# Kernel optimization log

Hardware: AMD Instinct MI355X
Metric: run time of the kernel (lower is better)

The kernel has to match this reference:

```python
import jax, jax.numpy as jnp
import numpy as np

B, S, D, E, K = 4, 2048, 1024, 8, 2
H = 4 * D  # SwiGLU hidden size


def setup_inputs() -> dict:
    key = jax.random.key(0)
    ks = jax.random.split(key, 6)
    s = 0.02
    return {
        "x": jax.random.normal(ks[0], (B, S, D), dtype=jnp.float32),
        "Wr": jax.random.normal(ks[1], (D, E), dtype=jnp.float32) * s,
        "br": jnp.zeros((E,), jnp.float32),
        "Wg": jax.random.normal(ks[2], (E, D, H), dtype=jnp.float32) * s,
        "bg": jnp.zeros((E, H), jnp.float32),
        "Wu": jax.random.normal(ks[3], (E, D, H), dtype=jnp.float32) * s,
        "bu": jnp.zeros((E, H), jnp.float32),
        "Wd": jax.random.normal(ks[4], (E, H, D), dtype=jnp.float32) * s,
        "bd": jnp.zeros((E, D), jnp.float32),
        "top_k": K,
    }


def reference(x, Wr, br, Wg, bg, Wu, bu, Wd, bd, top_k):
    # Router: top-k over expert logits, softmax over the selected k values.
    Bx, Sx, Dx = x.shape
    Ex = Wr.shape[-1]
    logits = x @ Wr + br                              # [B,S,E]
    vals, idx = jax.lax.top_k(logits, top_k)          # [B,S,K]
    probs = jax.nn.softmax(vals, axis=-1)             # [B,S,K]
    # Dense per-token expert weight; 0 for experts the token is not routed to.
    gate_w = jnp.sum(jax.nn.one_hot(idx, Ex, dtype=x.dtype) * probs[..., None], axis=-2)  # [B,S,E]

    xt = x.reshape(-1, Dx)          # [T,D]
    gw = gate_w.reshape(-1, Ex).T   # [E,T]

    def body(acc, p):
        wg, bgi, wu, bui, wd, bdi, ge = p
        h = jax.nn.silu(xt @ wg + bgi) * (xt @ wu + bui)   # [T,4D]
        y = (h @ wd + bdi) * ge[:, None]                   # zero where ge==0 (not routed)
        return acc + y, None

    out, _ = jax.lax.scan(body, jnp.zeros_like(xt), (Wg, bg, Wu, bu, Wd, bd, gw))
    return out.reshape(Bx, Sx, Dx)
```

## Files before the change

kernel.cpp:

```cpp
#include <hip/hip_runtime.h>
#include <hip/hip_fp16.h>


#define T_TOK 8192
#define D_IN  1024
#define E_EXP 8
#define H_HID 4096
#define NSLOT (T_TOK * 2)
#define NSLOT_PAD (NSLOT + 256)

typedef _Float16 f16;
typedef __attribute__((ext_vector_type(8))) _Float16 f16x8;
typedef __attribute__((ext_vector_type(4))) _Float16 f16x4;
typedef __attribute__((ext_vector_type(4))) float f32x4;

__device__ __forceinline__ void gload_lds16(const void* g, void* l) {
  __builtin_amdgcn_global_load_lds(
      (const __attribute__((address_space(1))) unsigned int*)g,
      (__attribute__((address_space(3))) unsigned int*)l, 16, 0, 0);
}


__global__ __launch_bounds__(256) void convert_x_kernel(
    const float* __restrict__ x, f16* __restrict__ xb, int n4) {
  int i = blockIdx.x * 256 + threadIdx.x;
  if (i >= n4) return;
  float4 v = ((const float4*)x)[i];
  f16x4 o = {(f16)v.x, (f16)v.y, (f16)v.z, (f16)v.w};
  *(f16x4*)(xb + (size_t)i * 4) = o;
}

template<int MAP>
__global__ __launch_bounds__(256) void transpose_cvt_kernel(
    const float* __restrict__ src, f16* __restrict__ dst, int R, int C,
    size_t dstride) {
  __shared__ float tile[32][33];
  int b = blockIdx.z;
  const float* s = src + (size_t)b * R * C;
  f16* d = dst + (size_t)b * dstride;
  int c0 = blockIdx.x * 32, r0 = blockIdx.y * 32;
  int tr = threadIdx.x >> 3;
  int tc4 = (threadIdx.x & 7) * 4;
  float4 v = *(const float4*)(s + (size_t)(r0 + tr) * C + c0 + tc4);
  tile[tr][tc4 + 0] = v.x;
  tile[tr][tc4 + 1] = v.y;
  tile[tr][tc4 + 2] = v.z;
  tile[tr][tc4 + 3] = v.w;
  __syncthreads();
  int c = c0 + tr;
  int ro = (MAP == 0) ? c : (((c >> 4) << 5) + ((MAP == 2) ? 16 : 0) + (c & 15));
  f16x4 o = {(f16)tile[tc4 + 0][tr], (f16)tile[tc4 + 1][tr],
             (f16)tile[tc4 + 2][tr], (f16)tile[tc4 + 3][tr]};
  *(f16x4*)(d + (size_t)ro * R + r0 + tc4) = o;
}


__global__ __launch_bounds__(256) void router_kernel(
    const float* __restrict__ x, const float* __restrict__ Wr,
    const float* __restrict__ br, int* __restrict__ eidx,
    float2* __restrict__ pval, int* __restrict__ counts) {
  int lane = threadIdx.x & 63, wid = threadIdx.x >> 6;
  int t = blockIdx.x * 4 + wid;
  const float* xr = x + (size_t)t * D_IN;
  float s[8] = {0.f, 0.f, 0.f, 0.f, 0.f, 0.f, 0.f, 0.f};
  int dbase = lane * 16;
#pragma unroll
  for (int i = 0; i < 4; ++i) {
    float4 xv = *(const float4*)(xr + dbase + i * 4);
    const float xs[4] = {xv.x, xv.y, xv.z, xv.w};
#pragma unroll
    for (int j = 0; j < 4; ++j) {
      const float* wr = Wr + (size_t)(dbase + i * 4 + j) * E_EXP;
      float4 w0 = *(const float4*)wr;
      float4 w1 = *(const float4*)(wr + 4);
      float xvj = xs[j];
      s[0] += xvj * w0.x; s[1] += xvj * w0.y; s[2] += xvj * w0.z; s[3] += xvj * w0.w;
      s[4] += xvj * w1.x; s[5] += xvj * w1.y; s[6] += xvj * w1.z; s[7] += xvj * w1.w;
    }
  }
#pragma unroll
  for (int off = 32; off; off >>= 1)
#pragma unroll
    for (int e = 0; e < 8; ++e) s[e] += __shfl_xor(s[e], off);
  if (lane == 0) {
    float v[8];
#pragma unroll
    for (int e = 0; e < 8; ++e) v[e] = s[e] + br[e];
    int i0 = 0; float v0 = v[0];
#pragma unroll
    for (int e = 1; e < 8; ++e) if (v[e] > v0) { v0 = v[e]; i0 = e; }
    int i1 = -1; float v1 = -1e30f;
#pragma unroll
    for (int e = 0; e < 8; ++e)
      if (e != i0 && v[e] > v1) { v1 = v[e]; i1 = e; }
    float ed = __expf(v1 - v0);
    float inv = 1.f / (1.f + ed);
    eidx[t] = i0 | (i1 << 8);
    pval[t] = make_float2(inv, ed * inv);
    atomicAdd(&counts[i0], 1);
    atomicAdd(&counts[i1], 1);
  }
}

__global__ void scan_kernel(const int* __restrict__ counts, int* __restrict__ offsets) {
  if (threadIdx.x == 0) {
    int acc = 0;
#pragma unroll
    for (int e = 0; e < E_EXP; ++e) { offsets[e] = acc; acc += counts[e]; }
    offsets[E_EXP] = acc;
  }
}

__global__ __launch_bounds__(256) void scatter_kernel(
    const int* __restrict__ eidx, const float2* __restrict__ pval,
    const int* __restrict__ offsets, int* __restrict__ cursors,
    int* __restrict__ perm, float* __restrict__ gatew, int2* __restrict__ slotAB) {
  int t = blockIdx.x * 256 + threadIdx.x;
  if (t >= T_TOK) return;
  int ei = eidx[t];
  float2 p = pval[t];
  int e0 = ei & 0xff, e1 = (ei >> 8) & 0xff;
  int s0 = offsets[e0] + atomicAdd(&cursors[e0], 1);
  perm[s0] = t; gatew[s0] = p.x;
  int s1 = offsets[e1] + atomicAdd(&cursors[e1], 1);
  perm[s1] = t; gatew[s1] = p.y;
  slotAB[t] = make_int2(s0, s1);
}


#define SB0 __builtin_amdgcn_sched_barrier(0)
#define BAR do { SB0; __builtin_amdgcn_s_barrier(); SB0; } while (0)

#define STAGE_(B, ISB, H, KT, BASE) do {                                   \
  char* d_ = smem + (B)*65536 + (ISB)*32768 + (H)*16384 + wid*1024;        \
  gload_lds16(BASE[(H)*2+0] + (size_t)(KT)*64, d_);                        \
  gload_lds16(BASE[(H)*2+1] + (size_t)(KT)*64, d_ + 8192);                 \
} while (0)

#define LDA_(B, Q)                                                          \
  _Pragma("unroll")                                                         \
  for (int m_ = 0; m_ < 4; ++m_) {                                          \
    fa[m_][0] = *(const f16x8*)(smem + (B)*65536 + aoff + ((Q)*4+m_)*2048 + offk0); \
    fa[m_][1] = *(const f16x8*)(smem + (B)*65536 + aoff + ((Q)*4+m_)*2048 + offk1); \
  }

#define LDB_(FB, B, RH)                                                     \
  _Pragma("unroll")                                                         \
  for (int n_ = 0; n_ < 2; ++n_) {                                          \
    FB[n_][0] = *(const f16x8*)(smem + (B)*65536 + 32768 + boff + ((RH)*2+n_)*2048 + offk0); \
    FB[n_][1] = *(const f16x8*)(smem + (B)*65536 + 32768 + boff + ((RH)*2+n_)*2048 + offk1); \
  }

#define QUAD_(Q, RH, FB)                                                    \
  __builtin_amdgcn_s_setprio(1);                                            \
  _Pragma("unroll")                                                         \
  for (int m_ = 0; m_ < 4; ++m_)                                            \
    _Pragma("unroll")                                                       \
    for (int n_ = 0; n_ < 2; ++n_) {                                        \
      acc[(Q)*4+m_][(RH)*2+n_] = __builtin_amdgcn_mfma_f32_16x16x32_f16(    \
          fa[m_][0], FB[n_][0], acc[(Q)*4+m_][(RH)*2+n_], 0, 0, 0);         \
      acc[(Q)*4+m_][(RH)*2+n_] = __builtin_amdgcn_mfma_f32_16x16x32_f16(    \
          fa[m_][1], FB[n_][1], acc[(Q)*4+m_][(RH)*2+n_], 0, 0, 0);         \
    }                                                                       \
  __builtin_amdgcn_s_setprio(0);

template<int MODE>
__global__ __launch_bounds__(512, 2) void ffn_8ph_kernel(
    const f16* __restrict__ Asrc, const f16* __restrict__ Bsrc,
    const float* __restrict__ bias0, const float* __restrict__ bias1,
    const int* __restrict__ offsets, const int* __restrict__ perm,
    const float* __restrict__ gatew, f16* __restrict__ dst) {
  constexpr int KD = MODE ? H_HID : D_IN;
  constexpr int BROWS = MODE ? D_IN : 2 * H_HID;
  constexpr int NT = KD / 64;
  static_assert(NT % 2 == 0, "NT even");

  __shared__ __align__(16) char smem[131072];

  int nt = blockIdx.x, e = blockIdx.y, mt = blockIdx.z;
  int off = offsets[e];
  int cnt = offsets[e + 1] - off;
  if (mt * 256 >= cnt) return;

  int tid = threadIdx.x, lane = tid & 63, wid = tid >> 6;
  int wm = wid >> 2, wn = wid & 3;
  int l15 = lane & 15, lc0 = lane >> 4, s7 = l15 & 7;
  int aoff = (wm * 128 + l15) * 128;
  int boff = (wn * 64 + l15) * 128;
  int offk0 = ((lc0) ^ s7) * 16;
  int offk1 = ((lc0 + 4) ^ s7) * 16;

  const f16 *aB[4], *bB[4];
#pragma unroll
  for (int h = 0; h < 2; ++h)
#pragma unroll
    for (int i = 0; i < 2; ++i) {
      int chunk = (i * 8 + wid) * 64 + lane;
      int rowh = chunk >> 3;
      int lc = (chunk & 7) ^ (rowh & 7);
      int absrow = h * 128 + rowh;
      int slot = off + min(mt * 256 + absrow, cnt - 1);
      if constexpr (MODE == 0)
        aB[h * 2 + i] = Asrc + (size_t)perm[slot] * KD + lc * 8;
      else
        aB[h * 2 + i] = Asrc + (size_t)slot * KD + lc * 8;
      bB[h * 2 + i] = Bsrc + ((size_t)e * BROWS + nt * 256 + absrow) * KD + lc * 8;
    }

  f32x4 acc[8][4] = {};
  f16x8 fa[4][2], fb01[2][2], fb23[2][2];

  STAGE_(0, 1, 0, 0, bB); STAGE_(0, 1, 1, 0, bB);
  STAGE_(0, 0, 0, 0, aB); STAGE_(0, 0, 1, 0, aB);
  STAGE_(1, 1, 0, 1, bB); STAGE_(1, 1, 1, 1, bB);
  asm volatile("s_waitcnt vmcnt(4)" ::: "memory");
  BAR;

  for (int it = 0; it < NT / 2; ++it) {
    int t1 = 2 * it + 1;
    int t2 = min(2 * it + 2, NT - 1);
    int t3 = min(2 * it + 3, NT - 1);
    LDA_(0, 0); LDB_(fb01, 0, 0); STAGE_(1, 0, 0, t1, aB);
    BAR; QUAD_(0, 0, fb01); BAR;
    LDB_(fb23, 0, 1); STAGE_(1, 0, 1, t1, aB);
    BAR; QUAD_(0, 1, fb23); BAR;
    LDA_(0, 1); STAGE_(0, 1, 0, t2, bB);
    BAR; QUAD_(1, 0, fb01); BAR;
    STAGE_(0, 1, 1, t2, bB);
    asm volatile("s_waitcnt vmcnt(4)" ::: "memory");
    BAR; QUAD_(1, 1, fb23); BAR;
    LDA_(1, 0); LDB_(fb01, 1, 0); STAGE_(0, 0, 0, t2, aB);
    BAR; QUAD_(0, 0, fb01); BAR;
    LDB_(fb23, 1, 1); STAGE_(0, 0, 1, t2, aB);
    BAR; QUAD_(0, 1, fb23); BAR;
    LDA_(1, 1); STAGE_(1, 1, 0, t3, bB);
    BAR; QUAD_(1, 0, fb01); BAR;
    STAGE_(1, 1, 1, t3, bB);
    asm volatile("s_waitcnt vmcnt(4)" ::: "memory");
    BAR; QUAD_(1, 1, fb23); BAR;
  }

  asm volatile("s_waitcnt vmcnt(0)" ::: "memory");
  BAR;

  int c0_ = lc0 * 4;
  if constexpr (MODE == 0) {
#pragma unroll
    for (int p = 0; p < 2; ++p) {
      int h = nt * 128 + wn * 32 + p * 16 + l15;
      float bgv = bias0[e * H_HID + h];
      float buv = bias1[e * H_HID + h];
#pragma unroll
      for (int m = 0; m < 8; ++m) {
        int lbase = mt * 256 + wm * 128 + m * 16 + c0_;
#pragma unroll
        for (int r = 0; r < 4; ++r) {
          if (lbase + r < cnt) {
            float g = acc[m][2 * p][r] + bgv;
            float u = acc[m][2 * p + 1][r] + buv;
            dst[(size_t)(off + lbase + r) * H_HID + h] =
                (f16)((g / (1.f + __expf(-g))) * u);
          }
        }
      }
    }
  } else {
#pragma unroll
    for (int n = 0; n < 4; ++n) {
      int col = nt * 256 + wn * 64 + n * 16 + l15;
      float bdv = bias0[e * D_IN + col];
#pragma unroll
      for (int m = 0; m < 8; ++m) {
        int lbase = mt * 256 + wm * 128 + m * 16 + c0_;
#pragma unroll
        for (int r = 0; r < 4; ++r) {
          if (lbase + r < cnt) {
            int slot = off + lbase + r;
            dst[(size_t)slot * D_IN + col] = (f16)(gatew[slot] * (acc[m][n][r] + bdv));
          }
        }
      }
    }
  }
}

__global__ __launch_bounds__(256) void combine_kernel(
    const f16* __restrict__ ybuf, const int2* __restrict__ slotAB,
    float* __restrict__ out) {
  int i = blockIdx.x * 256 + threadIdx.x;
  int t = i >> 7;
  int c8 = i & 127;
  int2 s = slotAB[t];
  f16x8 y0 = *(const f16x8*)(ybuf + (size_t)s.x * D_IN + c8 * 8);
  f16x8 y1 = *(const f16x8*)(ybuf + (size_t)s.y * D_IN + c8 * 8);
  float* o = out + (size_t)t * D_IN + c8 * 8;
  float4 o0 = make_float4((float)y0[0] + (float)y1[0], (float)y0[1] + (float)y1[1],
                          (float)y0[2] + (float)y1[2], (float)y0[3] + (float)y1[3]);
  float4 o1 = make_float4((float)y0[4] + (float)y1[4], (float)y0[5] + (float)y1[5],
                          (float)y0[6] + (float)y1[6], (float)y0[7] + (float)y1[7]);
  ((float4*)o)[0] = o0;
  ((float4*)o)[1] = o1;
}


extern "C" void kernel_launch(void* const* d_in, const int* in_sizes, int n_in,
                              void* d_out, int out_size, void* d_ws, size_t ws_size,
                              hipStream_t stream) {
  const float* x  = (const float*)d_in[0];
  const float* Wr = (const float*)d_in[1];
  const float* br = (const float*)d_in[2];
  const float* Wg = (const float*)d_in[3];
  const float* bg = (const float*)d_in[4];
  const float* Wu = (const float*)d_in[5];
  const float* bu = (const float*)d_in[6];
  const float* Wd = (const float*)d_in[7];
  const float* bd = (const float*)d_in[8];
  float* out = (float*)d_out;

  char* ws = (char*)d_ws;
  size_t o = 0;
  auto alloc = [&](size_t bytes) {
    size_t r = o;
    o += (bytes + 255) & ~(size_t)255;
    return r;
  };
  f16* xb     = (f16*)(ws + alloc((size_t)T_TOK * D_IN * 2));
  f16* wgut   = (f16*)(ws + alloc((size_t)E_EXP * 2 * H_HID * D_IN * 2));
  f16* wdt    = (f16*)(ws + alloc((size_t)E_EXP * D_IN * H_HID * 2));
  f16* hbuf   = (f16*)(ws + alloc((size_t)NSLOT_PAD * H_HID * 2));
  int* eidx   = (int*)(ws + alloc((size_t)T_TOK * 4));
  float2* pval= (float2*)(ws + alloc((size_t)T_TOK * 8));
  int* counts = (int*)(ws + alloc(64 * 4));
  int* cursors = counts + 8;
  int* offsets = counts + 16;
  int* perm   = (int*)(ws + alloc((size_t)NSLOT_PAD * 4));
  float* gatew= (float*)(ws + alloc((size_t)NSLOT_PAD * 4));
  int2* slotAB= (int2*)(ws + alloc((size_t)T_TOK * 8));
  f16* ybuf   = wgut;

  hipMemsetAsync(counts, 0, 64 * 4, stream);

  convert_x_kernel<<<(T_TOK * D_IN / 4 + 255) / 256, 256, 0, stream>>>(
      x, xb, T_TOK * D_IN / 4);
  transpose_cvt_kernel<1><<<dim3(H_HID / 32, D_IN / 32, E_EXP), 256, 0, stream>>>(
      Wg, wgut, D_IN, H_HID, (size_t)2 * H_HID * D_IN);
  transpose_cvt_kernel<2><<<dim3(H_HID / 32, D_IN / 32, E_EXP), 256, 0, stream>>>(
      Wu, wgut, D_IN, H_HID, (size_t)2 * H_HID * D_IN);
  transpose_cvt_kernel<0><<<dim3(D_IN / 32, H_HID / 32, E_EXP), 256, 0, stream>>>(
      Wd, wdt, H_HID, D_IN, (size_t)D_IN * H_HID);
  router_kernel<<<T_TOK / 4, 256, 0, stream>>>(x, Wr, br, eidx, pval, counts);
  scan_kernel<<<1, 64, 0, stream>>>(counts, offsets);
  scatter_kernel<<<T_TOK / 256, 256, 0, stream>>>(eidx, pval, offsets, cursors,
                                                  perm, gatew, slotAB);
  ffn_8ph_kernel<0><<<dim3(2 * H_HID / 256, E_EXP, 32), 512, 0, stream>>>(
      xb, wgut, bg, bu, offsets, perm, nullptr, hbuf);
  ffn_8ph_kernel<1><<<dim3(D_IN / 256, E_EXP, 32), 512, 0, stream>>>(
      hbuf, wdt, bd, nullptr, offsets, nullptr, gatew, ybuf);
  combine_kernel<<<T_TOK * D_IN / 8 / 256, 256, 0, stream>>>(ybuf, slotAB, out);
}
```

Before: 1.054 ms.

## Make gate/up FFN persistent per expert column tile and XCD-swizzle down-proj grid

The gate/up kernel now launches one block per (expert, N-tile), 256 blocks in total. Each block loops over all of that expert's M tiles, replacing the old 3D grid that launched many early-exiting blocks. The down-projection kernel uses a flat 1024-block grid whose index is remapped so that blocks sharing an expert's weight tiles land on the same XCD, which should improve L2 reuse. Biases are hoisted out of the M loop. The risk is load imbalance: each gate/up block runs serially over a variable number of tiles, so a heavily loaded expert sets the critical path.

```diff
diff --git a/kernel.cpp b/kernel.cpp
--- a/kernel.cpp
+++ b/kernel.cpp
@@ -177,10 +177,20 @@
 
   __shared__ __align__(16) char smem[131072];
 
-  int nt = blockIdx.x, e = blockIdx.y, mt = blockIdx.z;
+  int e, nt, mt0, mt1;
+  int g = blockIdx.x;
+  if constexpr (MODE == 0) {
+    e = g >> 5; nt = g & 31;
+  } else {
+    int xcd = g & 7, r = g >> 3;
+    int pair = xcd + 8 * (r & 3);
+    e = pair >> 2; nt = pair & 3; mt0 = r >> 2;
+  }
   int off = offsets[e];
   int cnt = offsets[e + 1] - off;
-  if (mt * 256 >= cnt) return;
+  int ntiles = (cnt + 255) >> 8;
+  if constexpr (MODE == 0) { mt0 = 0; mt1 = ntiles; }
+  else { if (mt0 >= ntiles) return; mt1 = mt0 + 1; }
 
   int tid = threadIdx.x, lane = tid & 63, wid = tid >> 6;
   int wm = wid >> 2, wn = wid & 3;
@@ -190,93 +200,119 @@
   int offk0 = ((lc0) ^ s7) * 16;
   int offk1 = ((lc0 + 4) ^ s7) * 16;
 
-  const f16 *aB[4], *bB[4];
+  int rowh_[2], lc_[2];
+#pragma unroll
+  for (int i = 0; i < 2; ++i) {
+    int chunk = (i * 8 + wid) * 64 + lane;
+    rowh_[i] = chunk >> 3;
+    lc_[i] = (chunk & 7) ^ (rowh_[i] & 7);
+  }
+
+  const f16* bB[4];
 #pragma unroll
   for (int h = 0; h < 2; ++h)
 #pragma unroll
-    for (int i = 0; i < 2; ++i) {
-      int chunk = (i * 8 + wid) * 64 + lane;
-      int rowh = chunk >> 3;
-      int lc = (chunk & 7) ^ (rowh & 7);
-      int absrow = h * 128 + rowh;
-      int slot = off + min(mt * 256 + absrow, cnt - 1);
-      if constexpr (MODE == 0)
-        aB[h * 2 + i] = Asrc + (size_t)perm[slot] * KD + lc * 8;
-      else
-        aB[h * 2 + i] = Asrc + (size_t)slot * KD + lc * 8;
-      bB[h * 2 + i] = Bsrc + ((size_t)e * BROWS + nt * 256 + absrow) * KD + lc * 8;
-    }
-
-  f32x4 acc[8][4] = {};
-  f16x8 fa[4][2], fb01[2][2], fb23[2][2];
-
-  STAGE_(0, 1, 0, 0, bB); STAGE_(0, 1, 1, 0, bB);
-  STAGE_(0, 0, 0, 0, aB); STAGE_(0, 0, 1, 0, aB);
-  STAGE_(1, 1, 0, 1, bB); STAGE_(1, 1, 1, 1, bB);
-  asm volatile("s_waitcnt vmcnt(4)" ::: "memory");
-  BAR;
-
-  for (int it = 0; it < NT / 2; ++it) {
-    int t1 = 2 * it + 1;
-    int t2 = min(2 * it + 2, NT - 1);
-    int t3 = min(2 * it + 3, NT - 1);
-    LDA_(0, 0); LDB_(fb01, 0, 0); STAGE_(1, 0, 0, t1, aB);
-    BAR; QUAD_(0, 0, fb01); BAR;
-    LDB_(fb23, 0, 1); STAGE_(1, 0, 1, t1, aB);
-    BAR; QUAD_(0, 1, fb23); BAR;
-    LDA_(0, 1); STAGE_(0, 1, 0, t2, bB);
-    BAR; QUAD_(1, 0, fb01); BAR;
-    STAGE_(0, 1, 1, t2, bB);
-    asm volatile("s_waitcnt vmcnt(4)" ::: "memory");
-    BAR; QUAD_(1, 1, fb23); BAR;
-    LDA_(1, 0); LDB_(fb01, 1, 0); STAGE_(0, 0, 0, t2, aB);
-    BAR; QUAD_(0, 0, fb01); BAR;
-    LDB_(fb23, 1, 1); STAGE_(0, 0, 1, t2, aB);
-    BAR; QUAD_(0, 1, fb23); BAR;
-    LDA_(1, 1); STAGE_(1, 1, 0, t3, bB);
-    BAR; QUAD_(1, 0, fb01); BAR;
-    STAGE_(1, 1, 1, t3, bB);
-    asm volatile("s_waitcnt vmcnt(4)" ::: "memory");
-    BAR; QUAD_(1, 1, fb23); BAR;
-  }
-
-  asm volatile("s_waitcnt vmcnt(0)" ::: "memory");
-  BAR;
-
-  int c0_ = lc0 * 4;
+    for (int i = 0; i < 2; ++i)
+      bB[h * 2 + i] =
+          Bsrc + ((size_t)e * BROWS + nt * 256 + h * 128 + rowh_[i]) * KD + lc_[i] * 8;
+
+  float bv0[4], bv1[2];
   if constexpr (MODE == 0) {
 #pragma unroll
     for (int p = 0; p < 2; ++p) {
       int h = nt * 128 + wn * 32 + p * 16 + l15;
-      float bgv = bias0[e * H_HID + h];
-      float buv = bias1[e * H_HID + h];
-#pragma unroll
-      for (int m = 0; m < 8; ++m) {
-        int lbase = mt * 256 + wm * 128 + m * 16 + c0_;
-#pragma unroll
-        for (int r = 0; r < 4; ++r) {
-          if (lbase + r < cnt) {
-            float g = acc[m][2 * p][r] + bgv;
-            float u = acc[m][2 * p + 1][r] + buv;
-            dst[(size_t)(off + lbase + r) * H_HID + h] =
-                (f16)((g / (1.f + __expf(-g))) * u);
+      bv0[p] = bias0[e * H_HID + h];
+      bv1[p] = bias1[e * H_HID + h];
+    }
+  } else {
+#pragma unroll
+    for (int n = 0; n < 4; ++n)
+      bv0[n] = bias0[e * D_IN + nt * 256 + wn * 64 + n * 16 + l15];
+  }
+
+  for (int mt = mt0; mt < mt1; ++mt) {
+    const f16* aB[4];
+#pragma unroll
+    for (int h = 0; h < 2; ++h)
+#pragma unroll
+      for (int i = 0; i < 2; ++i) {
+        int absrow = h * 128 + rowh_[i];
+        int slot = off + min(mt * 256 + absrow, cnt - 1);
+        if constexpr (MODE == 0)
+          aB[h * 2 + i] = Asrc + (size_t)perm[slot] * KD + lc_[i] * 8;
+        else
+          aB[h * 2 + i] = Asrc + (size_t)slot * KD + lc_[i] * 8;
+      }
+
+    f32x4 acc[8][4] = {};
+    f16x8 fa[4][2], fb01[2][2], fb23[2][2];
+
+    STAGE_(0, 1, 0, 0, bB); STAGE_(0, 1, 1, 0, bB);
+    STAGE_(0, 0, 0, 0, aB); STAGE_(0, 0, 1, 0, aB);
+    STAGE_(1, 1, 0, 1, bB); STAGE_(1, 1, 1, 1, bB);
+    asm volatile("s_waitcnt vmcnt(4)" ::: "memory");
+    BAR;
+
+    for (int it = 0; it < NT / 2; ++it) {
+      int t1 = 2 * it + 1;
+      int t2 = min(2 * it + 2, NT - 1);
+      int t3 = min(2 * it + 3, NT - 1);
+      LDA_(0, 0); LDB_(fb01, 0, 0); STAGE_(1, 0, 0, t1, aB);
+      BAR; QUAD_(0, 0, fb01); BAR;
+      LDB_(fb23, 0, 1); STAGE_(1, 0, 1, t1, aB);
+      BAR; QUAD_(0, 1, fb23); BAR;
+      LDA_(0, 1); STAGE_(0, 1, 0, t2, bB);
+      BAR; QUAD_(1, 0, fb01); BAR;
+      STAGE_(0, 1, 1, t2, bB);
+      asm volatile("s_waitcnt vmcnt(4)" ::: "memory");
+      BAR; QUAD_(1, 1, fb23); BAR;
+      LDA_(1, 0); LDB_(fb01, 1, 0); STAGE_(0, 0, 0, t2, aB);
+      BAR; QUAD_(0, 0, fb01); BAR;
+      LDB_(fb23, 1, 1); STAGE_(0, 0, 1, t2, aB);
+      BAR; QUAD_(0, 1, fb23); BAR;
+      LDA_(1, 1); STAGE_(1, 1, 0, t3, bB);
+      BAR; QUAD_(1, 0, fb01); BAR;
+      STAGE_(1, 1, 1, t3, bB);
+      asm volatile("s_waitcnt vmcnt(4)" ::: "memory");
+      BAR; QUAD_(1, 1, fb23); BAR;
+    }
+
+    asm volatile("s_waitcnt vmcnt(0)" ::: "memory");
+    BAR;
+
+    int c0_ = lc0 * 4;
+    if constexpr (MODE == 0) {
+#pragma unroll
+      for (int p = 0; p < 2; ++p) {
+        int h = nt * 128 + wn * 32 + p * 16 + l15;
+#pragma unroll
+        for (int m = 0; m < 8; ++m) {
+          int lbase = mt * 256 + wm * 128 + m * 16 + c0_;
+#pragma unroll
+          for (int r = 0; r < 4; ++r) {
+            if (lbase + r < cnt) {
+              float gv = acc[m][2 * p][r] + bv0[p];
+              float uv = acc[m][2 * p + 1][r] + bv1[p];
+              dst[(size_t)(off + lbase + r) * H_HID + h] =
+                  (f16)((gv / (1.f + __expf(-gv))) * uv);
+            }
           }
         }
       }
-    }
-  } else {
-#pragma unroll
-    for (int n = 0; n < 4; ++n) {
-      int col = nt * 256 + wn * 64 + n * 16 + l15;
-      float bdv = bias0[e * D_IN + col];
-#pragma unroll
-      for (int m = 0; m < 8; ++m) {
-        int lbase = mt * 256 + wm * 128 + m * 16 + c0_;
-#pragma unroll
-        for (int r = 0; r < 4; ++r) {
-          if (lbase + r < cnt) {
-            int slot = off + lbase + r;
-            dst[(size_t)slot * D_IN + col] = (f16)(gatew[slot] * (acc[m][n][r] + bdv));
+    } else {
+#pragma unroll
+      for (int n = 0; n < 4; ++n) {
+        int col = nt * 256 + wn * 64 + n * 16 + l15;
+#pragma unroll
+        for (int m = 0; m < 8; ++m) {
+          int lbase = mt * 256 + wm * 128 + m * 16 + c0_;
+#pragma unroll
+          for (int r = 0; r < 4; ++r) {
+            if (lbase + r < cnt) {
+              int slot = off + lbase + r;
+              dst[(size_t)slot * D_IN + col] =
+                  (f16)(gatew[slot] * (acc[m][n][r] + bv0[n]));
+            }
           }
         }
       }
@@ -352,9 +388,9 @@
   scan_kernel<<<1, 64, 0, stream>>>(counts, offsets);
   scatter_kernel<<<T_TOK / 256, 256, 0, stream>>>(eidx, pval, offsets, cursors,
                                                   perm, gatew, slotAB);
-  ffn_8ph_kernel<0><<<dim3(2 * H_HID / 256, E_EXP, 32), 512, 0, stream>>>(
+  ffn_8ph_kernel<0><<<dim3(E_EXP * 32), 512, 0, stream>>>(
       xb, wgut, bg, bu, offsets, perm, nullptr, hbuf);
-  ffn_8ph_kernel<1><<<dim3(D_IN / 256, E_EXP, 32), 512, 0, stream>>>(
+  ffn_8ph_kernel<1><<<dim3(1024), 512, 0, stream>>>(
       hbuf, wdt, bd, nullptr, offsets, nullptr, gatew, ybuf);
   combine_kernel<<<T_TOK * D_IN / 8 / 256, 256, 0, stream>>>(ybuf, slotAB, out);
 }
```

After: 1.109 ms. 1.05x slower.
